# Kernel optimization log

Measured on AMD Instinct MI355X. Metric: run time of the kernel, lower is better.

## Reference

```python
import jax, jax.numpy as jnp
import numpy as np

B, S, E, H = 2, 2048, 2048, 16
D = E // H  # head_dim = 128


def _rope_tables(seq_len, dim):
    # standard RoPE: theta_i = 10000^(-2i/dim), angles duplicated over pair halves
    inv_freq = 1.0 / (10000.0 ** (np.arange(0, dim, 2, dtype=np.float32) / dim))
    angles = np.arange(seq_len, dtype=np.float32)[:, None] * inv_freq[None, :]  # [S, D/2]
    angles = np.concatenate([angles, angles], axis=-1)  # [S, D]
    return jnp.asarray(np.cos(angles)), jnp.asarray(np.sin(angles))


def setup_inputs() -> dict:
    key = jax.random.key(0)
    ks = jax.random.split(key, 10)
    sc = 1.0 / np.sqrt(E)
    cos, sin = _rope_tables(S, D)
    mask = jnp.tril(jnp.ones((S, S), dtype=bool))[None, None]  # causal [1,1,S,S]
    return {
        "x_q": jax.random.normal(ks[0], (B, S, E), jnp.float32),
        "x_kv": jax.random.normal(ks[1], (B, S, E), jnp.float32),
        "cos": cos,
        "sin": sin,
        "wq": jax.random.normal(ks[2], (E, E), jnp.float32) * sc,
        "bq": jax.random.normal(ks[3], (E,), jnp.float32) * 0.01,
        "wk": jax.random.normal(ks[4], (E, E), jnp.float32) * sc,
        "bk": jax.random.normal(ks[5], (E,), jnp.float32) * 0.01,
        "wv": jax.random.normal(ks[6], (E, E), jnp.float32) * sc,
        "bv": jax.random.normal(ks[7], (E,), jnp.float32) * 0.01,
        "wo": jax.random.normal(ks[8], (E, E), jnp.float32) * sc,
        "bo": jax.random.normal(ks[9], (E,), jnp.float32) * 0.01,
        "mask": mask,
    }


def _apply_rope(x, cos, sin):
    # x: [B,H,S,D]; cos/sin: [S,D]. rotate-half convention.
    x1, x2 = jnp.split(x, 2, axis=-1)
    rot = jnp.concatenate([-x2, x1], axis=-1)
    return x * cos[None, None] + rot * sin[None, None]


def reference(x_q, x_kv, cos, sin, wq, bq, wk, bk, wv, bv, wo, bo, mask):
    b, sq, _ = x_q.shape
    skv = x_kv.shape[1]
    q = (x_q @ wq.T + bq).reshape(b, sq, H, D).transpose(0, 2, 1, 3)   # [B,H,Sq,D]
    k = (x_kv @ wk.T + bk).reshape(b, skv, H, D).transpose(0, 2, 1, 3)
    v = (x_kv @ wv.T + bv).reshape(b, skv, H, D).transpose(0, 2, 1, 3)
    q = _apply_rope(q, cos, sin)
    k = _apply_rope(k, cos, sin)
    scores = jnp.einsum("bhqd,bhkd->bhqk", q, k) / jnp.sqrt(jnp.float32(D))
    scores = jnp.where(mask, scores, jnp.float32(-1e9))
    w = jax.nn.softmax(scores, axis=-1)  # dropout p=0 -> identity
    out = jnp.einsum("bhqk,bhkd->bhqd", w, v)
    out = out.transpose(0, 2, 1, 3).reshape(b, sq, H * D)
    return out @ wo.T + bo
```

## Files before the change

kernel.cpp:

```cpp
#include <hip/hip_runtime.h>
#include <hip/hip_bf16.h>

#define Bb 2
#define Ss 2048
#define Ee 2048
#define Hh 16
#define Dd 128
#define Mrows (Bb*Ss)

typedef short short8 __attribute__((ext_vector_type(8)));
typedef float f32x4 __attribute__((ext_vector_type(4)));

__device__ __forceinline__ unsigned short bf_rne(float f) {
    unsigned u = __builtin_bit_cast(unsigned, f);
    u += 0x7fffu + ((u >> 16) & 1u);
    return (unsigned short)(u >> 16);
}
__device__ __forceinline__ float bf2f(unsigned short x) {
    unsigned u = ((unsigned)x) << 16;
    return __builtin_bit_cast(float, u);
}
__device__ __forceinline__ void load_lds16(const void* g, void* l) {
    __builtin_amdgcn_global_load_lds(
        (const __attribute__((address_space(1))) unsigned int*)g,
        (__attribute__((address_space(3))) unsigned int*)l, 16, 0, 0);
}

__global__ void cast_all_kernel(const float4* __restrict__ xq, const float4* __restrict__ xkv,
                                const float4* __restrict__ wq, const float4* __restrict__ wk,
                                const float4* __restrict__ wv, const float4* __restrict__ wo,
                                ushort4* __restrict__ out) {
    int i = blockIdx.x * 256 + threadIdx.x;
    const float4* src;
    int rel;
    if (i < 2097152)       { src = xq;  rel = i; }
    else if (i < 4194304)  { src = xkv; rel = i - 2097152; }
    else if (i < 5242880)  { src = wq;  rel = i - 4194304; }
    else if (i < 6291456)  { src = wk;  rel = i - 5242880; }
    else if (i < 7340032)  { src = wv;  rel = i - 6291456; }
    else                   { src = wo;  rel = i - 7340032; }
    float4 v = src[rel];
    ushort4 o;
    o.x = bf_rne(v.x); o.y = bf_rne(v.y); o.z = bf_rne(v.z); o.w = bf_rne(v.w);
    out[i] = o;
}

__device__ __forceinline__ void gemm_core(
    const short* __restrict__ A, const short* __restrict__ W, int K,
    int m0, int n0, int wave, int lane, short* As, short* Bs, f32x4 acc[4][4])
{
    const int wm = (wave & 1) * 64;
    const int wn = (wave >> 1) * 64;
    const int quad = lane >> 4;
    const int l16  = lane & 15;
    const int lrow   = lane >> 3;
    const int gchunk = (lane & 7) ^ lrow;

    for (int kt = 0; kt < K; kt += 64) {
        __syncthreads();
        #pragma unroll
        for (int j = 0; j < 4; ++j) {
            int row = wave*32 + j*8 + lrow;
            load_lds16(A + (size_t)(m0 + row)*K + kt + gchunk*8, &As[(wave*32 + j*8)*64]);
            load_lds16(W + (size_t)(n0 + row)*K + kt + gchunk*8, &Bs[(wave*32 + j*8)*64]);
        }
        __syncthreads();

        #pragma unroll
        for (int ks = 0; ks < 64; ks += 32) {
            const int cs = ks >> 3;
            short8 af[4], bfr[4];
            #pragma unroll
            for (int i = 0; i < 4; ++i)
                af[i] = *(const short8*)&As[(wm + i*16 + l16)*64 + (((cs + quad) ^ (l16 & 7)) << 3)];
            #pragma unroll
            for (int j = 0; j < 4; ++j)
                bfr[j] = *(const short8*)&Bs[(wn + j*16 + l16)*64 + (((cs + quad) ^ (l16 & 7)) << 3)];
            #pragma unroll
            for (int i = 0; i < 4; ++i)
                #pragma unroll
                for (int j = 0; j < 4; ++j)
                    acc[i][j] = __builtin_amdgcn_mfma_f32_16x16x32_bf16(af[i], bfr[j], acc[i][j], 0, 0, 0);
        }
    }
}

union GemmSmem {
    struct { short As[128*64]; short Bs[128*64]; } st;
    short T[128*137];
};

__global__ __launch_bounds__(256) void qkv_gemm(
    const short* __restrict__ xq, const short* __restrict__ xkv,
    const short* __restrict__ wq, const short* __restrict__ wk, const short* __restrict__ wv,
    const float* __restrict__ bq, const float* __restrict__ bk, const float* __restrict__ bv,
    short* __restrict__ Qr, short* __restrict__ Kr, short* __restrict__ VT)
{
    __shared__ GemmSmem sm;
    const int tid  = threadIdx.x;
    const int wave = tid >> 6;
    const int lane = tid & 63;
    const int quad = lane >> 4;
    const int l16  = lane & 15;
    const int m0   = blockIdx.x * 128;
    const int sub  = blockIdx.y >> 4;
    const int nb   = blockIdx.y & 15;
    const int n0   = nb * 128;
    const int wm = (wave & 1) * 64;
    const int wn = (wave >> 1) * 64;

    const short* A = (sub == 0) ? xq : xkv;
    const short* W = (sub == 0) ? wq : (sub == 1) ? wk : wv;
    const float* bias = (sub == 0) ? bq : (sub == 1) ? bk : bv;

    f32x4 acc[4][4] = {};
    gemm_core(A, W, Ee, m0, n0, wave, lane, sm.st.As, sm.st.Bs, acc);

    const int b0 = m0 >> 11;
    const int s0 = m0 & (Ss - 1);

    if (sub < 2) {
        short* out = (sub == 0) ? Qr : Kr;
        #pragma unroll
        for (int i = 0; i < 4; ++i)
            #pragma unroll
            for (int j = 0; j < 4; ++j)
                #pragma unroll
                for (int r = 0; r < 4; ++r) {
                    int gm = m0 + wm + i*16 + quad*4 + r;
                    int gn = n0 + wn + j*16 + l16;
                    float v = acc[i][j][r] + bias[gn];
                    int b = gm >> 11, s = gm & (Ss-1);
                    int h = gn >> 7,  d = gn & (Dd-1);
                    out[(((size_t)(b*Hh + h)) * Ss + s) * Dd + d] = (short)bf_rne(v);
                }
    } else {
        __syncthreads();
        #pragma unroll
        for (int i = 0; i < 4; ++i)
            #pragma unroll
            for (int j = 0; j < 4; ++j)
                #pragma unroll
                for (int r = 0; r < 4; ++r) {
                    int ml = wm + i*16 + quad*4 + r;
                    int nl = wn + j*16 + l16;
                    sm.T[ml*137 + nl] = (short)bf_rne(acc[i][j][r] + bias[n0 + nl]);
                }
        __syncthreads();
        const int g = tid & 15, dbase = tid >> 4;
        const int h = nb;
        #pragma unroll
        for (int dd = 0; dd < 8; ++dd) {
            int d = dbase + dd*16;
            short8 v;
            #pragma unroll
            for (int c = 0; c < 8; ++c)
                v[c] = sm.T[(g*8 + c)*137 + d];
            *(short8*)&VT[(((size_t)(b0*Hh + h)) * Dd + d) * Ss + s0 + g*8] = v;
        }
    }
}

__global__ __launch_bounds__(256) void oproj_gemm(
    const short* __restrict__ A, const short* __restrict__ W,
    const float* __restrict__ bias, float* __restrict__ Cf)
{
    __shared__ GemmSmem sm;
    const int tid  = threadIdx.x;
    const int wave = tid >> 6;
    const int lane = tid & 63;
    const int quad = lane >> 4;
    const int l16  = lane & 15;
    const int m0 = blockIdx.x * 128;
    const int n0 = blockIdx.y * 128;
    const int wm = (wave & 1) * 64;
    const int wn = (wave >> 1) * 64;

    f32x4 acc[4][4] = {};
    gemm_core(A, W, Ee, m0, n0, wave, lane, sm.st.As, sm.st.Bs, acc);

    #pragma unroll
    for (int i = 0; i < 4; ++i)
        #pragma unroll
        for (int j = 0; j < 4; ++j)
            #pragma unroll
            for (int r = 0; r < 4; ++r) {
                int gm = m0 + wm + i*16 + quad*4 + r;
                int gn = n0 + wn + j*16 + l16;
                Cf[(size_t)gm * Ee + gn] = acc[i][j][r] + bias[gn];
            }
}

__global__ void rope_kernel(short* __restrict__ Qr, short* __restrict__ Kr,
                            const float* __restrict__ cosT, const float* __restrict__ sinT) {
    short* X    = blockIdx.y ? Kr : Qr;
    float scale = blockIdx.y ? 1.0f : 0.08838834764831845f;
    int idx = blockIdx.x * 256 + threadIdx.x;
    int d  = idx & 63;
    int s  = (idx >> 6) & (Ss - 1);
    int bh = idx >> 17;
    size_t base = ((size_t)bh * Ss + s) * Dd;
    float x1 = bf2f((unsigned short)X[base + d]);
    float x2 = bf2f((unsigned short)X[base + d + 64]);
    float c  = cosT[s*Dd + d];
    float sn = sinT[s*Dd + d];
    X[base + d]      = (short)bf_rne((x1 * c - x2 * sn) * scale);
    X[base + d + 64] = (short)bf_rne((x2 * c + x1 * sn) * scale);
}

__global__ __launch_bounds__(256, 2) void attn_kernel(
    const short* __restrict__ Q, const short* __restrict__ Kk,
    const short* __restrict__ VT, short* __restrict__ O)
{
    __shared__ short Ks[64*128];
    __shared__ short Vt[2][128*64];
    __shared__ short Pw[4][32*72];

    const int tid  = threadIdx.x;
    const int wave = tid >> 6;
    const int lane = tid & 63;
    const int quad = lane >> 4;
    const int l16  = lane & 15;
    const int mmap = (blockIdx.x + blockIdx.y) & 15;
    const int qt   = (blockIdx.y & 16) ? (15 - mmap) : mmap;
    const int bh = blockIdx.y;
    const int b  = bh >> 4, h = bh & 15;
    const size_t head_off = (size_t)bh * Ss * Dd;
    const short* Kg  = Kk + head_off;
    const short* VTg = VT + head_off;

    auto stageK = [&](int kt) {
        #pragma unroll
        for (int j = 0; j < 4; ++j) {
            int r = wave*16 + j*4 + (lane >> 4);
            int c = (lane & 15) ^ (r & 15);
            load_lds16(Kg + (size_t)(kt*64 + r)*Dd + c*8, &Ks[(wave*16 + j*4)*128]);
        }
    };
    auto stageV = [&](int kt, int buf) {
        #pragma unroll
        for (int j = 0; j < 4; ++j) {
            int r = wave*32 + j*8 + (lane >> 3);
            int c = (lane & 7) ^ (r & 7);
            load_lds16(VTg + (size_t)r*Ss + kt*64 + c*8, &Vt[buf][(wave*32 + j*8)*64]);
        }
    };

    const int qbase = qt*128 + wave*32;
    short8 qf[2][4];
    #pragma unroll
    for (int mi = 0; mi < 2; ++mi)
        #pragma unroll
        for (int ds = 0; ds < 4; ++ds)
            qf[mi][ds] = *(const short8*)&Q[head_off + (size_t)(qbase + mi*16 + l16)*Dd + ds*32 + quad*8];

    f32x4 o[2][8] = {};
    float m_i[2][4], l_i[2][4];
    #pragma unroll
    for (int mi = 0; mi < 2; ++mi)
        #pragma unroll
        for (int r = 0; r < 4; ++r) { m_i[mi][r] = -__builtin_inff(); l_i[mi][r] = 0.f; }

    const int ktiles = 2*qt + 2;
    stageK(0);
    stageV(0, 0);

    for (int kt = 0; kt < ktiles; ++kt) {
        __syncthreads();
        if (kt + 1 < ktiles) stageV(kt+1, (kt+1)&1);

        f32x4 sc[2][4] = {};
        #pragma unroll
        for (int jk = 0; jk < 4; ++jk)
            #pragma unroll
            for (int ds = 0; ds < 4; ++ds) {
                short8 kf = *(const short8*)&Ks[(jk*16 + l16)*128 + (((ds*4 + quad) ^ l16) * 8)];
                #pragma unroll
                for (int mi = 0; mi < 2; ++mi)
                    sc[mi][jk] = __builtin_amdgcn_mfma_f32_16x16x32_bf16(qf[mi][ds], kf, sc[mi][jk], 0, 0, 0);
            }

        __syncthreads();
        if (kt + 1 < ktiles) stageK(kt+1);

        const int k0 = kt*64;
        #pragma unroll
        for (int mi = 0; mi < 2; ++mi) {
            if (k0 + 63 > qbase + mi*16) {
                #pragma unroll
                for (int jk = 0; jk < 4; ++jk) {
                    int kg = k0 + jk*16 + l16;
                    #pragma unroll
                    for (int r = 0; r < 4; ++r)
                        if (kg > qbase + mi*16 + quad*4 + r) sc[mi][jk][r] = -__builtin_inff();
                }
            }
        }

        float alpha[2][4];
        #pragma unroll
        for (int mi = 0; mi < 2; ++mi)
            #pragma unroll
            for (int r = 0; r < 4; ++r) {
                float mx = fmaxf(fmaxf(sc[mi][0][r], sc[mi][1][r]), fmaxf(sc[mi][2][r], sc[mi][3][r]));
                #pragma unroll
                for (int off = 1; off < 16; off <<= 1)
                    mx = fmaxf(mx, __shfl_xor(mx, off));
                float mn = fmaxf(m_i[mi][r], mx);
                alpha[mi][r] = __expf(m_i[mi][r] - mn);
                m_i[mi][r] = mn;
                float s = 0.f;
                #pragma unroll
                for (int jk = 0; jk < 4; ++jk) {
                    float p = __expf(sc[mi][jk][r] - mn);
                    sc[mi][jk][r] = p;
                    s += p;
                }
                l_i[mi][r] = l_i[mi][r] * alpha[mi][r] + s;
            }

        #pragma unroll
        for (int mi = 0; mi < 2; ++mi)
            #pragma unroll
            for (int jk = 0; jk < 4; ++jk)
                #pragma unroll
                for (int r = 0; r < 4; ++r)
                    Pw[wave][(mi*16 + quad*4 + r)*72 + jk*16 + l16] = (short)bf_rne(sc[mi][jk][r]);

        #pragma unroll
        for (int mi = 0; mi < 2; ++mi)
            #pragma unroll
            for (int dt = 0; dt < 8; ++dt)
                #pragma unroll
                for (int r = 0; r < 4; ++r)
                    o[mi][dt][r] *= alpha[mi][r];

        short8 pa[2][2];
        #pragma unroll
        for (int mi = 0; mi < 2; ++mi)
            #pragma unroll
            for (int kk = 0; kk < 2; ++kk)
                pa[mi][kk] = *(const short8*)&Pw[wave][(mi*16 + l16)*72 + kk*32 + quad*8];

        const short* vb = Vt[kt & 1];
        #pragma unroll
        for (int dt = 0; dt < 8; ++dt)
            #pragma unroll
            for (int kk = 0; kk < 2; ++kk) {
                short8 vf = *(const short8*)&vb[(dt*16 + l16)*64 + (((kk*4 + quad) ^ (l16 & 7)) * 8)];
                #pragma unroll
                for (int mi = 0; mi < 2; ++mi)
                    o[mi][dt] = __builtin_amdgcn_mfma_f32_16x16x32_bf16(pa[mi][kk], vf, o[mi][dt], 0, 0, 0);
            }
    }

    #pragma unroll
    for (int mi = 0; mi < 2; ++mi)
        #pragma unroll
        for (int r = 0; r < 4; ++r) {
            float l = l_i[mi][r];
            #pragma unroll
            for (int off = 1; off < 16; off <<= 1)
                l += __shfl_xor(l, off);
            float inv = 1.0f / l;
            int srow = qbase + mi*16 + quad*4 + r;
            size_t obase = ((size_t)b * Ss + srow) * Ee + h * Dd;
            #pragma unroll
            for (int dt = 0; dt < 8; ++dt)
                O[obase + dt*16 + l16] = (short)bf_rne(o[mi][dt][r] * inv);
        }
}

extern "C" void kernel_launch(void* const* d_in, const int* in_sizes, int n_in,
                              void* d_out, int out_size, void* d_ws, size_t ws_size,
                              hipStream_t stream) {
    const float* x_q  = (const float*)d_in[0];
    const float* x_kv = (const float*)d_in[1];
    const float* cosT = (const float*)d_in[2];
    const float* sinT = (const float*)d_in[3];
    const float* wq = (const float*)d_in[4];
    const float* bq = (const float*)d_in[5];
    const float* wk = (const float*)d_in[6];
    const float* bk = (const float*)d_in[7];
    const float* wv = (const float*)d_in[8];
    const float* bv = (const float*)d_in[9];
    const float* wo = (const float*)d_in[10];
    const float* bo = (const float*)d_in[11];

    size_t off = 0;
    auto alloc = [&](size_t bytes) {
        void* p = (char*)d_ws + off;
        off += (bytes + 255) & ~(size_t)255;
        return p;
    };
    const size_t nX = (size_t)Mrows * Ee;
    const size_t nW = (size_t)Ee * Ee;
    short* xq16  = (short*)alloc(nX * 2);
    short* xkv16 = (short*)alloc(nX * 2);
    short* wq16  = (short*)alloc(nW * 2);
    short* wk16  = (short*)alloc(nW * 2);
    short* wv16  = (short*)alloc(nW * 2);
    short* wo16  = (short*)alloc(nW * 2);
    short* Qr    = (short*)alloc(nX * 2);
    short* Kr    = (short*)alloc(nX * 2);
    short* VTb   = (short*)alloc(nX * 2);
    short* Ob    = (short*)alloc(nX * 2);

    cast_all_kernel<<<32768, 256, 0, stream>>>(
        (const float4*)x_q, (const float4*)x_kv, (const float4*)wq,
        (const float4*)wk, (const float4*)wv, (const float4*)wo, (ushort4*)xq16);

    qkv_gemm<<<dim3(Mrows/128, 48), 256, 0, stream>>>(
        xq16, xkv16, wq16, wk16, wv16, bq, bk, bv, Qr, Kr, VTb);

    rope_kernel<<<dim3((Bb*Hh*Ss*64)/256, 2), 256, 0, stream>>>(Qr, Kr, cosT, sinT);

    attn_kernel<<<dim3(16, Bb*Hh), 256, 0, stream>>>(Qr, Kr, VTb, Ob);

    oproj_gemm<<<dim3(Mrows/128, Ee/128), 256, 0, stream>>>(Ob, wo16, bo, (float*)d_out);
}
```

Baseline: 456.4 us.

## Triple-buffer GEMM LDS pipeline with 256x128 tiles and raw waitcnt barriers

Rewrites the shared GEMM core to use 256x128 block tiles with K-step 32 and a three-stage LDS ring buffer. Global-to-LDS loads for tile t+2 are issued while tile t is computed, and synchronisation uses s_waitcnt vmcnt plus s_barrier instead of two __syncthreads per step. Each wave now holds a 128x64 accumulator (8x4 MFMA tiles), with s_setprio raised around the MFMA burst. The V-transpose epilogue is reworked to use per-wave LDS tiles. This aims to hide global load latency and raise MFMA density, at the cost of more registers and 72KB of LDS per block, which may limit occupancy, and it halves the grid size.

```diff
diff --git a/kernel.cpp b/kernel.cpp
--- a/kernel.cpp
+++ b/kernel.cpp
@@ -45,148 +45,156 @@
     out[i] = o;
 }
 
+#define NTK 64
+#define BUFB 24576
+
 __device__ __forceinline__ void gemm_core(
-    const short* __restrict__ A, const short* __restrict__ W, int K,
-    int m0, int n0, int wave, int lane, short* As, short* Bs, f32x4 acc[4][4])
+    const short* __restrict__ A, const short* __restrict__ W,
+    int m0, int n0, char* lds, f32x4 (&acc)[8][4], int tid)
 {
-    const int wm = (wave & 1) * 64;
-    const int wn = (wave >> 1) * 64;
-    const int quad = lane >> 4;
-    const int l16  = lane & 15;
-    const int lrow   = lane >> 3;
-    const int gchunk = (lane & 7) ^ lrow;
-
-    for (int kt = 0; kt < K; kt += 64) {
-        __syncthreads();
-        #pragma unroll
-        for (int j = 0; j < 4; ++j) {
-            int row = wave*32 + j*8 + lrow;
-            load_lds16(A + (size_t)(m0 + row)*K + kt + gchunk*8, &As[(wave*32 + j*8)*64]);
-            load_lds16(W + (size_t)(n0 + row)*K + kt + gchunk*8, &Bs[(wave*32 + j*8)*64]);
-        }
-        __syncthreads();
-
-        #pragma unroll
-        for (int ks = 0; ks < 64; ks += 32) {
-            const int cs = ks >> 3;
-            short8 af[4], bfr[4];
-            #pragma unroll
-            for (int i = 0; i < 4; ++i)
-                af[i] = *(const short8*)&As[(wm + i*16 + l16)*64 + (((cs + quad) ^ (l16 & 7)) << 3)];
+    const int wid  = tid >> 6, lane = tid & 63;
+    const int wr   = wid >> 1, wc   = wid & 1;
+    const int quad = lane >> 4, l16 = lane & 15;
+    const int lr   = lane >> 3, sl  = lane & 7;
+    const int g    = sl ^ lr;
+    const int grow = 2*(wid*8 + lr) + (g >> 2);
+    const int kcol = (g & 3) * 8;
+    const int cx16 = ((((l16 & 1) << 2) + quad) ^ ((l16 >> 1) & 7)) << 4;
+    const int arow = (l16 >> 1) << 7;
+
+    const short* Ab = A + (size_t)(m0 + grow) * Ee + kcol;
+    const short* Wb = W + (size_t)(n0 + grow) * Ee + kcol;
+
+    auto stageTile = [&](int kt, int so) {
+        const short* a = Ab + kt * 32;
+        const short* w = Wb + kt * 32;
+        #pragma unroll
+        for (int i = 0; i < 4; ++i)
+            load_lds16(a + (size_t)i*64*Ee, lds + so + i*4096 + wid*1024);
+        #pragma unroll
+        for (int i = 0; i < 2; ++i)
+            load_lds16(w + (size_t)i*64*Ee, lds + so + 16384 + i*4096 + wid*1024);
+    };
+
+    stageTile(0, 0);
+    stageTile(1, BUFB);
+    asm volatile("s_waitcnt vmcnt(6)\n\ts_barrier" ::: "memory");
+
+    int bo = 0, so = 2*BUFB;
+    for (int t = 0; t < NTK; ++t) {
+        if (t + 2 < NTK) stageTile(t + 2, so);
+
+        const char* Abase = lds + bo + wr*8192 + arow + cx16;
+        const char* Bbase = lds + bo + 16384 + wc*4096 + arow + cx16;
+        short8 af[8], bf[4];
+        #pragma unroll
+        for (int i = 0; i < 8; ++i) af[i] = *(const short8*)(Abase + i*1024);
+        #pragma unroll
+        for (int j = 0; j < 4; ++j) bf[j] = *(const short8*)(Bbase + j*1024);
+
+        __builtin_amdgcn_s_setprio(1);
+        #pragma unroll
+        for (int i = 0; i < 8; ++i)
             #pragma unroll
             for (int j = 0; j < 4; ++j)
-                bfr[j] = *(const short8*)&Bs[(wn + j*16 + l16)*64 + (((cs + quad) ^ (l16 & 7)) << 3)];
-            #pragma unroll
-            for (int i = 0; i < 4; ++i)
-                #pragma unroll
-                for (int j = 0; j < 4; ++j)
-                    acc[i][j] = __builtin_amdgcn_mfma_f32_16x16x32_bf16(af[i], bfr[j], acc[i][j], 0, 0, 0);
-        }
+                acc[i][j] = __builtin_amdgcn_mfma_f32_16x16x32_bf16(af[i], bf[j], acc[i][j], 0, 0, 0);
+        __builtin_amdgcn_s_setprio(0);
+
+        if (t == NTK - 1) break;
+        if (t < NTK - 2) asm volatile("s_waitcnt vmcnt(6)\n\ts_barrier" ::: "memory");
+        else             asm volatile("s_waitcnt vmcnt(0)\n\ts_barrier" ::: "memory");
+        bo = (bo == 2*BUFB) ? 0 : bo + BUFB;
+        so = (so == 2*BUFB) ? 0 : so + BUFB;
     }
 }
 
-union GemmSmem {
-    struct { short As[128*64]; short Bs[128*64]; } st;
-    short T[128*137];
-};
-
-__global__ __launch_bounds__(256) void qkv_gemm(
+__global__ __launch_bounds__(256, 2) void qkv_gemm(
     const short* __restrict__ xq, const short* __restrict__ xkv,
     const short* __restrict__ wq, const short* __restrict__ wk, const short* __restrict__ wv,
     const float* __restrict__ bq, const float* __restrict__ bk, const float* __restrict__ bv,
     short* __restrict__ Qr, short* __restrict__ Kr, short* __restrict__ VT)
 {
-    __shared__ GemmSmem sm;
+    __shared__ __align__(16) char lds[73728];
     const int tid  = threadIdx.x;
-    const int wave = tid >> 6;
-    const int lane = tid & 63;
-    const int quad = lane >> 4;
-    const int l16  = lane & 15;
-    const int m0   = blockIdx.x * 128;
+    const int wid  = tid >> 6, lane = tid & 63;
+    const int quad = lane >> 4, l16 = lane & 15;
+    const int wr   = wid >> 1, wc   = wid & 1;
+    const int m0   = blockIdx.x * 256;
     const int sub  = blockIdx.y >> 4;
     const int nb   = blockIdx.y & 15;
     const int n0   = nb * 128;
-    const int wm = (wave & 1) * 64;
-    const int wn = (wave >> 1) * 64;
 
     const short* A = (sub == 0) ? xq : xkv;
     const short* W = (sub == 0) ? wq : (sub == 1) ? wk : wv;
     const float* bias = (sub == 0) ? bq : (sub == 1) ? bk : bv;
 
-    f32x4 acc[4][4] = {};
-    gemm_core(A, W, Ee, m0, n0, wave, lane, sm.st.As, sm.st.Bs, acc);
+    f32x4 acc[8][4] = {};
+    gemm_core(A, W, m0, n0, lds, acc, tid);
 
     const int b0 = m0 >> 11;
     const int s0 = m0 & (Ss - 1);
 
     if (sub < 2) {
-        short* out = (sub == 0) ? Qr : Kr;
-        #pragma unroll
-        for (int i = 0; i < 4; ++i)
+        short* out = sub ? Kr : Qr;
+        #pragma unroll
+        for (int i = 0; i < 8; ++i)
             #pragma unroll
             for (int j = 0; j < 4; ++j)
                 #pragma unroll
                 for (int r = 0; r < 4; ++r) {
-                    int gm = m0 + wm + i*16 + quad*4 + r;
-                    int gn = n0 + wn + j*16 + l16;
-                    float v = acc[i][j][r] + bias[gn];
-                    int b = gm >> 11, s = gm & (Ss-1);
-                    int h = gn >> 7,  d = gn & (Dd-1);
-                    out[(((size_t)(b*Hh + h)) * Ss + s) * Dd + d] = (short)bf_rne(v);
+                    int gm = m0 + wr*128 + i*16 + quad*4 + r;
+                    int d  = wc*64 + j*16 + l16;
+                    float v = acc[i][j][r] + bias[n0 + d];
+                    int b = gm >> 11, s = gm & (Ss - 1);
+                    out[(((size_t)(b*Hh + nb)) * Ss + s) * Dd + d] = (short)bf_rne(v);
                 }
     } else {
         __syncthreads();
-        #pragma unroll
-        for (int i = 0; i < 4; ++i)
+        short* T = (short*)lds + wid * 8704;
+        #pragma unroll
+        for (int i = 0; i < 8; ++i)
             #pragma unroll
             for (int j = 0; j < 4; ++j)
                 #pragma unroll
                 for (int r = 0; r < 4; ++r) {
-                    int ml = wm + i*16 + quad*4 + r;
-                    int nl = wn + j*16 + l16;
-                    sm.T[ml*137 + nl] = (short)bf_rne(acc[i][j][r] + bias[n0 + nl]);
+                    int dl  = j*16 + l16;
+                    int slc = i*16 + quad*4 + r;
+                    T[dl*136 + slc] = (short)bf_rne(acc[i][j][r] + bias[n0 + wc*64 + dl]);
                 }
         __syncthreads();
-        const int g = tid & 15, dbase = tid >> 4;
-        const int h = nb;
-        #pragma unroll
-        for (int dd = 0; dd < 8; ++dd) {
-            int d = dbase + dd*16;
-            short8 v;
-            #pragma unroll
-            for (int c = 0; c < 8; ++c)
-                v[c] = sm.T[(g*8 + c)*137 + d];
-            *(short8*)&VT[(((size_t)(b0*Hh + h)) * Dd + d) * Ss + s0 + g*8] = v;
+        #pragma unroll
+        for (int ss = 0; ss < 16; ++ss) {
+            short8 v = *(const short8*)&T[lane*136 + ss*8];
+            int dg = wc*64 + lane;
+            int sg = s0 + wr*128 + ss*8;
+            *(short8*)&VT[(((size_t)(b0*Hh + nb)) * Dd + dg) * Ss + sg] = v;
         }
     }
 }
 
-__global__ __launch_bounds__(256) void oproj_gemm(
+__global__ __launch_bounds__(256, 2) void oproj_gemm(
     const short* __restrict__ A, const short* __restrict__ W,
     const float* __restrict__ bias, float* __restrict__ Cf)
 {
-    __shared__ GemmSmem sm;
+    __shared__ __align__(16) char lds[73728];
     const int tid  = threadIdx.x;
-    const int wave = tid >> 6;
-    const int lane = tid & 63;
-    const int quad = lane >> 4;
-    const int l16  = lane & 15;
-    const int m0 = blockIdx.x * 128;
-    const int n0 = blockIdx.y * 128;
-    const int wm = (wave & 1) * 64;
-    const int wn = (wave >> 1) * 64;
-
-    f32x4 acc[4][4] = {};
-    gemm_core(A, W, Ee, m0, n0, wave, lane, sm.st.As, sm.st.Bs, acc);
+    const int wid  = tid >> 6, lane = tid & 63;
+    const int quad = lane >> 4, l16 = lane & 15;
+    const int wr   = wid >> 1, wc   = wid & 1;
+    const int m0   = blockIdx.x * 256;
+    const int n0   = blockIdx.y * 128;
+
+    f32x4 acc[8][4] = {};
+    gemm_core(A, W, m0, n0, lds, acc, tid);
 
     #pragma unroll
-    for (int i = 0; i < 4; ++i)
+    for (int i = 0; i < 8; ++i)
         #pragma unroll
         for (int j = 0; j < 4; ++j)
             #pragma unroll
             for (int r = 0; r < 4; ++r) {
-                int gm = m0 + wm + i*16 + quad*4 + r;
-                int gn = n0 + wn + j*16 + l16;
+                int gm = m0 + wr*128 + i*16 + quad*4 + r;
+                int gn = n0 + wc*64 + j*16 + l16;
                 Cf[(size_t)gm * Ee + gn] = acc[i][j][r] + bias[gn];
             }
 }
@@ -410,12 +418,12 @@
         (const float4*)x_q, (const float4*)x_kv, (const float4*)wq,
         (const float4*)wk, (const float4*)wv, (const float4*)wo, (ushort4*)xq16);
 
-    qkv_gemm<<<dim3(Mrows/128, 48), 256, 0, stream>>>(
+    qkv_gemm<<<dim3(Mrows/256, 48), 256, 0, stream>>>(
         xq16, xkv16, wq16, wk16, wv16, bq, bk, bv, Qr, Kr, VTb);
 
     rope_kernel<<<dim3((Bb*Hh*Ss*64)/256, 2), 256, 0, stream>>>(Qr, Kr, cosT, sinT);
 
     attn_kernel<<<dim3(16, Bb*Hh), 256, 0, stream>>>(Qr, Kr, VTb, Ob);
 
-    oproj_gemm<<<dim3(Mrows/128, Ee/128), 256, 0, stream>>>(Ob, wo16, bo, (float*)d_out);
-}
+    oproj_gemm<<<dim3(Mrows/256, Ee/128), 256, 0, stream>>>(Ob, wo16, bo, (float*)d_out);
+}
```

Measured after the change: 440.6 us. 3.5% less time.
